# Performance work log

Measured on AMD Instinct MI355X. Metric: run time of the kernel, lower is better.

The kernel has to match this reference:

```python
import jax, jax.numpy as jnp
import numpy as np

B, N, E, H = 4, 2048, 512, 8
D = E // H  # head dim = 64


def setup_inputs() -> dict:
    key = jax.random.key(0)
    ks = jax.random.split(key, 5)
    s = 1.0 / np.sqrt(E)
    return {
        "x": jax.random.normal(ks[0], (B, N, E), dtype=jnp.float32),
        "Wk": jax.random.normal(ks[1], (E, E), dtype=jnp.float32) * s,
        "bk": jax.random.normal(ks[2], (E,), dtype=jnp.float32) * s,
        "Wv": jax.random.normal(ks[3], (E, E), dtype=jnp.float32) * s,
        "bv": jax.random.normal(ks[4], (E,), dtype=jnp.float32) * s,
    }


def reference(x, Wk, bk, Wv, bv):
    b, n, e = x.shape
    # Linear projections (torch Linear: y = x @ W.T + b), split into heads.
    keys = (x @ Wk.T + bk).reshape(b, n, H, D).transpose(0, 2, 1, 3)    # b h n d
    values = (x @ Wv.T + bv).reshape(b, n, H, D).transpose(0, 2, 1, 3)  # b h n d
    # Q = K self-attention: scores [b, h, n, n]
    dotprod = jnp.einsum('bhnd,bhmd->bhnm', keys, keys)
    # softmax over last axis, then unusual POST-softmax scaling by sqrt(emb)
    att = jax.nn.softmax(dotprod, axis=-1) / jnp.sqrt(jnp.asarray(e, x.dtype))
    # dropout p=0 -> identity
    out = jnp.einsum('bhnm,bhmd->bhnd', att, values)
    return out.transpose(0, 2, 1, 3).reshape(b, n, e)
```

## Files before the change

### kernel.cpp

```cpp
#include <hip/hip_runtime.h>

typedef __bf16 bf16_t;
typedef bf16_t bf16x8 __attribute__((ext_vector_type(8)));
typedef float f32x4 __attribute__((ext_vector_type(4)));

#define NSEQ 2048
#define EMB 512
#define HEADS 8
#define HD 64
#define BATCH 4
#define LOG2E 1.4426950408889634f

#define MFMA16(a, b, c) __builtin_amdgcn_mfma_f32_16x16x32_bf16(a, b, c, 0, 0, 0)

#define CX (BATCH * NSEQ * EMB / 8)
#define CW (EMB * EMB / 8)
__global__ __launch_bounds__(256) void convert_kernel(
    const float* __restrict__ x, const float* __restrict__ Wk,
    const float* __restrict__ Wv,
    bf16_t* __restrict__ xb, bf16_t* __restrict__ Wb)
{
  const int total = CX + 2 * CW;
  for (int c = blockIdx.x * 256 + threadIdx.x; c < total; c += gridDim.x * 256) {
    const float* src;
    bf16_t* dst;
    int off;
    if (c < CX)            { src = x;  dst = xb;      off = c; }
    else if (c < CX + CW)  { src = Wk; dst = Wb;      off = c - CX; }
    else                   { src = Wv; dst = Wb + (size_t)EMB * EMB; off = c - CX - CW; }
    const float4 a = *(const float4*)(src + (size_t)off * 8);
    const float4 bq = *(const float4*)(src + (size_t)off * 8 + 4);
    bf16x8 v;
    v[0] = (bf16_t)a.x;  v[1] = (bf16_t)a.y;  v[2] = (bf16_t)a.z;  v[3] = (bf16_t)a.w;
    v[4] = (bf16_t)bq.x; v[5] = (bf16_t)bq.y; v[6] = (bf16_t)bq.z; v[7] = (bf16_t)bq.w;
    *(bf16x8*)(dst + (size_t)off * 8) = v;
  }
}

__global__ __launch_bounds__(256, 2) void proj_kernel(
    const bf16_t* __restrict__ xb, const bf16_t* __restrict__ Wb,
    const float* __restrict__ bk, const float* __restrict__ bv,
    bf16_t* __restrict__ Kh, bf16_t* __restrict__ Vt)
{
  __shared__ union {
    struct {
      __align__(16) bf16_t A[2][128][40];
      __align__(16) bf16_t B[2][128][40];
    } s;
    __align__(16) bf16_t T[128][136];
  } u;

  const int t    = threadIdx.x;
  const int w    = t >> 6;
  const int lane = t & 63;
  const int quad = lane >> 4;
  const int l15  = lane & 15;
  const int wr   = w >> 1, wc = w & 1;
  const int m0   = blockIdx.x * 128;
  const int n0   = blockIdx.y * 128;
  const int zz   = (blockIdx.y >= 4);

  const int sr = t >> 3;
  const int sj = t & 7;
  const int sb = sj >> 2, sc = (sj & 3) * 8;

  bf16x8 pa[4], pb[4];
  auto prefetch = [&](int k0) {
#pragma unroll
    for (int i = 0; i < 4; ++i) {
      pa[i] = *(const bf16x8*)(xb + (size_t)(m0 + sr + i * 32) * EMB + k0 + sj * 8);
      pb[i] = *(const bf16x8*)(Wb + (size_t)(n0 + sr + i * 32) * EMB + k0 + sj * 8);
    }
  };

  f32x4 acc[4][4] = {};
  prefetch(0);

  for (int it = 0; it < 8; ++it) {
    __syncthreads();
#pragma unroll
    for (int i = 0; i < 4; ++i) {
      *(bf16x8*)(&u.s.A[sb][sr + i * 32][sc]) = pa[i];
      *(bf16x8*)(&u.s.B[sb][sr + i * 32][sc]) = pb[i];
    }
    __syncthreads();
    if (it < 7) prefetch((it + 1) * 64);

    bf16x8 af[4][2], bf[4][2];
#pragma unroll
    for (int mt = 0; mt < 4; ++mt)
#pragma unroll
      for (int kk = 0; kk < 2; ++kk)
        af[mt][kk] = *(const bf16x8*)(&u.s.A[kk][wr * 64 + mt * 16 + l15][quad * 8]);
#pragma unroll
    for (int nt = 0; nt < 4; ++nt)
#pragma unroll
      for (int kk = 0; kk < 2; ++kk)
        bf[nt][kk] = *(const bf16x8*)(&u.s.B[kk][wc * 64 + nt * 16 + l15][quad * 8]);
#pragma unroll
    for (int kk = 0; kk < 2; ++kk)
#pragma unroll
      for (int mt = 0; mt < 4; ++mt)
#pragma unroll
        for (int nt = 0; nt < 4; ++nt)
          acc[mt][nt] = MFMA16(af[mt][kk], bf[nt][kk], acc[mt][nt]);
  }

  __syncthreads();

#pragma unroll
  for (int mt = 0; mt < 4; ++mt) {
#pragma unroll
    for (int nt = 0; nt < 4; ++nt) {
      const int F = wc * 64 + nt * 16 + l15;
      const int c = n0 + F;
      const float bb = zz ? bv[c - 512] : bk[c];
#pragma unroll
      for (int reg = 0; reg < 4; ++reg) {
        const int R = wr * 64 + mt * 16 + quad * 4 + reg;
        const float v = acc[mt][nt][reg] + bb;
        if (!zz) u.T[R][F] = (bf16_t)v;
        else     u.T[F][R] = (bf16_t)v;
      }
    }
  }
  __syncthreads();

#pragma unroll
  for (int i = 0; i < 8; ++i) {
    const int q  = t + i * 256;
    const int R  = q >> 4;
    const int C8 = (q & 15) * 8;
    const bf16x8 v = *(const bf16x8*)(&u.T[R][C8]);
    if (!zz) {
      const int gr = m0 + R, b = gr >> 11, n = gr & (NSEQ - 1);
      const int c = n0 + C8, hh = c >> 6, d = c & 63;
      *(bf16x8*)(Kh + (((size_t)(b * HEADS + hh)) * NSEQ + n) * HD + d) = v;
    } else {
      const int cv = n0 + R - 512, hh = cv >> 6, d = cv & 63;
      const int gr = m0 + C8, b = gr >> 11, n = gr & (NSEQ - 1);
      *(bf16x8*)(Vt + (((size_t)(b * HEADS + hh)) * HD + d) * NSEQ + n) = v;
    }
  }
}

__global__ __launch_bounds__(256, 2) void flash_kernel(
    const bf16_t* __restrict__ Kh, const bf16_t* __restrict__ Vt,
    float* __restrict__ out)
{
  __shared__ __align__(16) bf16_t Kl[2][64][40];
  __shared__ __align__(16) bf16_t Vl[2][64][40];
  __shared__ __align__(16) bf16_t Pl[4][32][68];

  const int t    = threadIdx.x;
  const int w    = t >> 6;
  const int lane = t & 63;
  const int quad = lane >> 4;
  const int l15  = lane & 15;

  const int bh = blockIdx.x;
  const int b  = bh >> 3, h = bh & 7;
  const int rowbase = blockIdx.y * 128 + w * 32;

  const bf16_t* __restrict__ Kb = Kh + (size_t)bh * NSEQ * HD;
  const bf16_t* __restrict__ Vb = Vt + (size_t)bh * HD * NSEQ;

  bf16x8 qf[2][2];
#pragma unroll
  for (int mt = 0; mt < 2; ++mt)
#pragma unroll
    for (int kk = 0; kk < 2; ++kk)
      qf[mt][kk] = *(const bf16x8*)(Kb + (size_t)(rowbase + mt * 16 + l15) * HD +
                                    kk * 32 + quad * 8);

  float mlog[2][4];
#pragma unroll
  for (int mt = 0; mt < 2; ++mt) {
    float ss = 0.f;
#pragma unroll
    for (int kk = 0; kk < 2; ++kk)
#pragma unroll
      for (int j = 0; j < 8; ++j) {
        const float qv = (float)qf[mt][kk][j];
        ss = fmaf(qv, qv, ss);
      }
    ss += __shfl_xor(ss, 16, 64);
    ss += __shfl_xor(ss, 32, 64);
#pragma unroll
    for (int reg = 0; reg < 4; ++reg)
      mlog[mt][reg] =
          __shfl(ss, (lane & 48) | (((lane >> 4) << 2) + reg), 64) * LOG2E;
  }

  const int sr = t >> 3, sj = t & 7;
  const int sb = sj >> 2, sc = (sj & 3) * 8;

  bf16x8 pk[2], pv[2];
  auto prefetch = [&](int kt) {
    const bf16_t* Kt = Kb + (size_t)kt * 64 * HD;
    pk[0] = *(const bf16x8*)(Kt + (size_t)sr * HD + sj * 8);
    pk[1] = *(const bf16x8*)(Kt + (size_t)(sr + 32) * HD + sj * 8);
    pv[0] = *(const bf16x8*)(Vb + (size_t)sr * NSEQ + kt * 64 + sj * 8);
    pv[1] = *(const bf16x8*)(Vb + (size_t)(sr + 32) * NSEQ + kt * 64 + sj * 8);
  };

  f32x4 acco[2][4] = {};
  float lsum[2][4] = {};

  prefetch(0);

  for (int kt = 0; kt < NSEQ / 64; ++kt) {
    __syncthreads();
    *(bf16x8*)(&Kl[sb][sr][sc])      = pk[0];
    *(bf16x8*)(&Kl[sb][sr + 32][sc]) = pk[1];
    *(bf16x8*)(&Vl[sb][sr][sc])      = pv[0];
    *(bf16x8*)(&Vl[sb][sr + 32][sc]) = pv[1];
    __syncthreads();
    if (kt + 1 < NSEQ / 64) prefetch(kt + 1);

    bf16x8 kf[4][2];
#pragma unroll
    for (int nt = 0; nt < 4; ++nt)
#pragma unroll
      for (int kk = 0; kk < 2; ++kk)
        kf[nt][kk] = *(const bf16x8*)(&Kl[kk][nt * 16 + l15][quad * 8]);

    f32x4 s[2][4] = {};
#pragma unroll
    for (int mt = 0; mt < 2; ++mt)
#pragma unroll
      for (int nt = 0; nt < 4; ++nt) {
        s[mt][nt] = MFMA16(qf[mt][0], kf[nt][0], s[mt][nt]);
        s[mt][nt] = MFMA16(qf[mt][1], kf[nt][1], s[mt][nt]);
      }

#pragma unroll
    for (int mt = 0; mt < 2; ++mt)
#pragma unroll
      for (int nt = 0; nt < 4; ++nt)
#pragma unroll
        for (int reg = 0; reg < 4; ++reg) {
          const float p =
              __builtin_amdgcn_exp2f(fmaf(s[mt][nt][reg], LOG2E, -mlog[mt][reg]));
          lsum[mt][reg] += p;
          Pl[w][mt * 16 + quad * 4 + reg][nt * 16 + l15] = (bf16_t)p;
        }

#pragma unroll
    for (int kk = 0; kk < 2; ++kk) {
      bf16x8 vfs[4];
#pragma unroll
      for (int dt = 0; dt < 4; ++dt)
        vfs[dt] = *(const bf16x8*)(&Vl[kk][dt * 16 + l15][quad * 8]);
#pragma unroll
      for (int mt = 0; mt < 2; ++mt) {
        const bf16x8 pf =
            *(const bf16x8*)(&Pl[w][mt * 16 + l15][kk * 32 + quad * 8]);
#pragma unroll
        for (int dt = 0; dt < 4; ++dt)
          acco[mt][dt] = MFMA16(pf, vfs[dt], acco[mt][dt]);
      }
    }
  }

#pragma unroll
  for (int mt = 0; mt < 2; ++mt)
#pragma unroll
    for (int off = 1; off <= 8; off <<= 1)
#pragma unroll
      for (int reg = 0; reg < 4; ++reg)
        lsum[mt][reg] += __shfl_xor(lsum[mt][reg], off, 64);

  const float SCL = 0.044194173824159216f;
#pragma unroll
  for (int mt = 0; mt < 2; ++mt)
#pragma unroll
    for (int dt = 0; dt < 4; ++dt) {
      const int d = dt * 16 + l15;
#pragma unroll
      for (int reg = 0; reg < 4; ++reg) {
        const int n = rowbase + mt * 16 + quad * 4 + reg;
        const float f = SCL / lsum[mt][reg];
        out[((size_t)(b * NSEQ + n)) * EMB + h * HD + d] = acco[mt][dt][reg] * f;
      }
    }
}

extern "C" void kernel_launch(void* const* d_in, const int* in_sizes, int n_in,
                              void* d_out, int out_size, void* d_ws, size_t ws_size,
                              hipStream_t stream) {
  const float* x  = (const float*)d_in[0];
  const float* Wk = (const float*)d_in[1];
  const float* bk = (const float*)d_in[2];
  const float* Wv = (const float*)d_in[3];
  const float* bv = (const float*)d_in[4];
  float* out = (float*)d_out;

  bf16_t* Kh = (bf16_t*)d_ws;
  bf16_t* Vt = Kh + (size_t)BATCH * HEADS * NSEQ * HD;
  bf16_t* xb = Vt + (size_t)BATCH * HEADS * NSEQ * HD;
  bf16_t* Wb = xb + (size_t)BATCH * NSEQ * EMB;

  convert_kernel<<<1024, 256, 0, stream>>>(x, Wk, Wv, xb, Wb);

  dim3 pg(8192 / 128, 1024 / 128);
  proj_kernel<<<pg, 256, 0, stream>>>(xb, Wb, bk, bv, Kh, Vt);

  dim3 fg(BATCH * HEADS, NSEQ / 128);
  flash_kernel<<<fg, 256, 0, stream>>>(Kh, Vt, out);
}
```

Baseline: 147.9 us.

## Fuse fp32-to-bf16 conversion into projection; split flash keys across waves

Removes the separate conversion kernel: the projection kernel now loads fp32 x and weights directly and packs them to bf16 before staging in shared memory, which saves a launch and one round trip through memory for x. The flash kernel is restructured so each wave owns 64 query rows and half of each 64-key tile. It computes transposed scores (K·Q), keeps one row-max per lane, and writes P with packed 8-byte stores. A final shared-memory reduction merges the two key-halves' partial outputs and sums. The cost is doubled fp32 global read traffic in the projection, since x is re-read by every column block, plus a cross-wave reduction at the end.

Result: faster. 133.6 us (-9.7%).

```diff
diff --git a/kernel.cpp b/kernel.cpp
--- a/kernel.cpp
+++ b/kernel.cpp
@@ -13,33 +13,10 @@
 
 #define MFMA16(a, b, c) __builtin_amdgcn_mfma_f32_16x16x32_bf16(a, b, c, 0, 0, 0)
 
-#define CX (BATCH * NSEQ * EMB / 8)
-#define CW (EMB * EMB / 8)
-__global__ __launch_bounds__(256) void convert_kernel(
-    const float* __restrict__ x, const float* __restrict__ Wk,
-    const float* __restrict__ Wv,
-    bf16_t* __restrict__ xb, bf16_t* __restrict__ Wb)
-{
-  const int total = CX + 2 * CW;
-  for (int c = blockIdx.x * 256 + threadIdx.x; c < total; c += gridDim.x * 256) {
-    const float* src;
-    bf16_t* dst;
-    int off;
-    if (c < CX)            { src = x;  dst = xb;      off = c; }
-    else if (c < CX + CW)  { src = Wk; dst = Wb;      off = c - CX; }
-    else                   { src = Wv; dst = Wb + (size_t)EMB * EMB; off = c - CX - CW; }
-    const float4 a = *(const float4*)(src + (size_t)off * 8);
-    const float4 bq = *(const float4*)(src + (size_t)off * 8 + 4);
-    bf16x8 v;
-    v[0] = (bf16_t)a.x;  v[1] = (bf16_t)a.y;  v[2] = (bf16_t)a.z;  v[3] = (bf16_t)a.w;
-    v[4] = (bf16_t)bq.x; v[5] = (bf16_t)bq.y; v[6] = (bf16_t)bq.z; v[7] = (bf16_t)bq.w;
-    *(bf16x8*)(dst + (size_t)off * 8) = v;
-  }
-}
-
 __global__ __launch_bounds__(256, 2) void proj_kernel(
-    const bf16_t* __restrict__ xb, const bf16_t* __restrict__ Wb,
-    const float* __restrict__ bk, const float* __restrict__ bv,
+    const float* __restrict__ x,
+    const float* __restrict__ Wk, const float* __restrict__ bk,
+    const float* __restrict__ Wv, const float* __restrict__ bv,
     bf16_t* __restrict__ Kh, bf16_t* __restrict__ Vt)
 {
   __shared__ union {
@@ -59,18 +36,28 @@
   const int m0   = blockIdx.x * 128;
   const int n0   = blockIdx.y * 128;
   const int zz   = (blockIdx.y >= 4);
+  const float* __restrict__ W = zz ? Wv : Wk;
+  const int nW = n0 - zz * 512;
 
   const int sr = t >> 3;
   const int sj = t & 7;
   const int sb = sj >> 2, sc = (sj & 3) * 8;
 
-  bf16x8 pa[4], pb[4];
+  float4 pa[4][2], pb[4][2];
   auto prefetch = [&](int k0) {
 #pragma unroll
     for (int i = 0; i < 4; ++i) {
-      pa[i] = *(const bf16x8*)(xb + (size_t)(m0 + sr + i * 32) * EMB + k0 + sj * 8);
-      pb[i] = *(const bf16x8*)(Wb + (size_t)(n0 + sr + i * 32) * EMB + k0 + sj * 8);
-    }
+      const float* xa = x + (size_t)(m0 + sr + i * 32) * EMB + k0 + sj * 8;
+      const float* wa = W + (size_t)(nW + sr + i * 32) * EMB + k0 + sj * 8;
+      pa[i][0] = *(const float4*)xa; pa[i][1] = *(const float4*)(xa + 4);
+      pb[i][0] = *(const float4*)wa; pb[i][1] = *(const float4*)(wa + 4);
+    }
+  };
+  auto pack8 = [](float4 a, float4 b) -> bf16x8 {
+    bf16x8 v;
+    v[0] = (bf16_t)a.x; v[1] = (bf16_t)a.y; v[2] = (bf16_t)a.z; v[3] = (bf16_t)a.w;
+    v[4] = (bf16_t)b.x; v[5] = (bf16_t)b.y; v[6] = (bf16_t)b.z; v[7] = (bf16_t)b.w;
+    return v;
   };
 
   f32x4 acc[4][4] = {};
@@ -80,8 +67,8 @@
     __syncthreads();
 #pragma unroll
     for (int i = 0; i < 4; ++i) {
-      *(bf16x8*)(&u.s.A[sb][sr + i * 32][sc]) = pa[i];
-      *(bf16x8*)(&u.s.B[sb][sr + i * 32][sc]) = pb[i];
+      *(bf16x8*)(&u.s.A[sb][sr + i * 32][sc]) = pack8(pa[i][0], pa[i][1]);
+      *(bf16x8*)(&u.s.B[sb][sr + i * 32][sc]) = pack8(pb[i][0], pb[i][1]);
     }
     __syncthreads();
     if (it < 7) prefetch((it + 1) * 64);
@@ -148,48 +135,55 @@
     const bf16_t* __restrict__ Kh, const bf16_t* __restrict__ Vt,
     float* __restrict__ out)
 {
-  __shared__ __align__(16) bf16_t Kl[2][64][40];
-  __shared__ __align__(16) bf16_t Vl[2][64][40];
-  __shared__ __align__(16) bf16_t Pl[4][32][68];
+  __shared__ union {
+    struct {
+      __align__(16) bf16_t Kl[2][64][40];
+      __align__(16) bf16_t Vl[2][64][40];
+      __align__(16) bf16_t Pl[4][64][40];
+    } s;
+    struct {
+      __align__(16) float Cb[2][4096];
+      __align__(16) float Lb[2][64][4];
+    } c;
+  } u;
 
   const int t    = threadIdx.x;
   const int w    = t >> 6;
   const int lane = t & 63;
   const int quad = lane >> 4;
   const int l15  = lane & 15;
+  const int rh   = w & 1;
+  const int kh   = w >> 1;
 
   const int bh = blockIdx.x;
   const int b  = bh >> 3, h = bh & 7;
-  const int rowbase = blockIdx.y * 128 + w * 32;
+  const int rowbase = blockIdx.y * 128 + rh * 64;
 
   const bf16_t* __restrict__ Kb = Kh + (size_t)bh * NSEQ * HD;
   const bf16_t* __restrict__ Vb = Vt + (size_t)bh * HD * NSEQ;
 
-  bf16x8 qf[2][2];
-#pragma unroll
-  for (int mt = 0; mt < 2; ++mt)
+  bf16x8 qf[4][2];
+#pragma unroll
+  for (int nt = 0; nt < 4; ++nt)
 #pragma unroll
     for (int kk = 0; kk < 2; ++kk)
-      qf[mt][kk] = *(const bf16x8*)(Kb + (size_t)(rowbase + mt * 16 + l15) * HD +
+      qf[nt][kk] = *(const bf16x8*)(Kb + (size_t)(rowbase + nt * 16 + l15) * HD +
                                     kk * 32 + quad * 8);
 
-  float mlog[2][4];
-#pragma unroll
-  for (int mt = 0; mt < 2; ++mt) {
+  float mlog[4];
+#pragma unroll
+  for (int nt = 0; nt < 4; ++nt) {
     float ss = 0.f;
 #pragma unroll
     for (int kk = 0; kk < 2; ++kk)
 #pragma unroll
       for (int j = 0; j < 8; ++j) {
-        const float qv = (float)qf[mt][kk][j];
+        const float qv = (float)qf[nt][kk][j];
         ss = fmaf(qv, qv, ss);
       }
     ss += __shfl_xor(ss, 16, 64);
     ss += __shfl_xor(ss, 32, 64);
-#pragma unroll
-    for (int reg = 0; reg < 4; ++reg)
-      mlog[mt][reg] =
-          __shfl(ss, (lane & 48) | (((lane >> 4) << 2) + reg), 64) * LOG2E;
+    mlog[nt] = ss * LOG2E;
   }
 
   const int sr = t >> 3, sj = t & 7;
@@ -204,86 +198,105 @@
     pv[1] = *(const bf16x8*)(Vb + (size_t)(sr + 32) * NSEQ + kt * 64 + sj * 8);
   };
 
-  f32x4 acco[2][4] = {};
-  float lsum[2][4] = {};
+  f32x4 acco[4][4] = {};
+  float lsum[4] = {0.f, 0.f, 0.f, 0.f};
 
   prefetch(0);
 
   for (int kt = 0; kt < NSEQ / 64; ++kt) {
     __syncthreads();
-    *(bf16x8*)(&Kl[sb][sr][sc])      = pk[0];
-    *(bf16x8*)(&Kl[sb][sr + 32][sc]) = pk[1];
-    *(bf16x8*)(&Vl[sb][sr][sc])      = pv[0];
-    *(bf16x8*)(&Vl[sb][sr + 32][sc]) = pv[1];
+    *(bf16x8*)(&u.s.Kl[sb][sr][sc])      = pk[0];
+    *(bf16x8*)(&u.s.Kl[sb][sr + 32][sc]) = pk[1];
+    *(bf16x8*)(&u.s.Vl[sb][sr][sc])      = pv[0];
+    *(bf16x8*)(&u.s.Vl[sb][sr + 32][sc]) = pv[1];
     __syncthreads();
     if (kt + 1 < NSEQ / 64) prefetch(kt + 1);
 
-    bf16x8 kf[4][2];
-#pragma unroll
-    for (int nt = 0; nt < 4; ++nt)
+    bf16x8 kf[2][2];
+#pragma unroll
+    for (int jt = 0; jt < 2; ++jt)
 #pragma unroll
       for (int kk = 0; kk < 2; ++kk)
-        kf[nt][kk] = *(const bf16x8*)(&Kl[kk][nt * 16 + l15][quad * 8]);
-
-    f32x4 s[2][4] = {};
-#pragma unroll
-    for (int mt = 0; mt < 2; ++mt)
+        kf[jt][kk] =
+            *(const bf16x8*)(&u.s.Kl[kk][kh * 32 + jt * 16 + l15][quad * 8]);
+
+    f32x4 st[2][4] = {};
+#pragma unroll
+    for (int kk = 0; kk < 2; ++kk)
+#pragma unroll
+      for (int jt = 0; jt < 2; ++jt)
+#pragma unroll
+        for (int nt = 0; nt < 4; ++nt)
+          st[jt][nt] = MFMA16(kf[jt][kk], qf[nt][kk], st[jt][nt]);
+
+#pragma unroll
+    for (int jt = 0; jt < 2; ++jt)
 #pragma unroll
       for (int nt = 0; nt < 4; ++nt) {
-        s[mt][nt] = MFMA16(qf[mt][0], kf[nt][0], s[mt][nt]);
-        s[mt][nt] = MFMA16(qf[mt][1], kf[nt][1], s[mt][nt]);
-      }
-
-#pragma unroll
-    for (int mt = 0; mt < 2; ++mt)
-#pragma unroll
-      for (int nt = 0; nt < 4; ++nt)
+        union { bf16_t hx[4]; uint2 u2; } pw;
 #pragma unroll
         for (int reg = 0; reg < 4; ++reg) {
           const float p =
-              __builtin_amdgcn_exp2f(fmaf(s[mt][nt][reg], LOG2E, -mlog[mt][reg]));
-          lsum[mt][reg] += p;
-          Pl[w][mt * 16 + quad * 4 + reg][nt * 16 + l15] = (bf16_t)p;
+              __builtin_amdgcn_exp2f(fmaf(st[jt][nt][reg], LOG2E, -mlog[nt]));
+          lsum[nt] += p;
+          pw.hx[reg] = (bf16_t)p;
         }
-
-#pragma unroll
-    for (int kk = 0; kk < 2; ++kk) {
-      bf16x8 vfs[4];
+        *(uint2*)(&u.s.Pl[w][nt * 16 + l15][jt * 16 + quad * 4]) = pw.u2;
+      }
+
+    bf16x8 vf[4];
+#pragma unroll
+    for (int dt = 0; dt < 4; ++dt)
+      vf[dt] = *(const bf16x8*)(&u.s.Vl[kh][dt * 16 + l15][quad * 8]);
+#pragma unroll
+    for (int rt = 0; rt < 4; ++rt) {
+      const bf16x8 pf = *(const bf16x8*)(&u.s.Pl[w][rt * 16 + l15][quad * 8]);
 #pragma unroll
       for (int dt = 0; dt < 4; ++dt)
-        vfs[dt] = *(const bf16x8*)(&Vl[kk][dt * 16 + l15][quad * 8]);
-#pragma unroll
-      for (int mt = 0; mt < 2; ++mt) {
-        const bf16x8 pf =
-            *(const bf16x8*)(&Pl[w][mt * 16 + l15][kk * 32 + quad * 8]);
+        acco[rt][dt] = MFMA16(pf, vf[dt], acco[rt][dt]);
+    }
+  }
+
+  __syncthreads();
+  if (kh == 1) {
+#pragma unroll
+    for (int rt = 0; rt < 4; ++rt)
+#pragma unroll
+      for (int dt = 0; dt < 4; ++dt)
+        *(f32x4*)(&u.c.Cb[rh][((rt * 4 + dt) * 64 + lane) * 4]) = acco[rt][dt];
+#pragma unroll
+    for (int nt = 0; nt < 4; ++nt) u.c.Lb[rh][lane][nt] = lsum[nt];
+  }
+  __syncthreads();
+  if (kh == 0) {
+#pragma unroll
+    for (int rt = 0; rt < 4; ++rt)
+#pragma unroll
+      for (int dt = 0; dt < 4; ++dt) {
+        const f32x4 o = *(const f32x4*)(&u.c.Cb[rh][((rt * 4 + dt) * 64 + lane) * 4]);
+        acco[rt][dt] += o;
+      }
+#pragma unroll
+    for (int nt = 0; nt < 4; ++nt) {
+      lsum[nt] += u.c.Lb[rh][lane][nt];
+      lsum[nt] += __shfl_xor(lsum[nt], 16, 64);
+      lsum[nt] += __shfl_xor(lsum[nt], 32, 64);
+    }
+
+    const float SCL = 0.044194173824159216f;
+#pragma unroll
+    for (int rt = 0; rt < 4; ++rt)
+#pragma unroll
+      for (int reg = 0; reg < 4; ++reg) {
+        const float lr = __shfl(lsum[rt], quad * 4 + reg, 64);
+        const float f = SCL / lr;
+        const int n = rowbase + rt * 16 + quad * 4 + reg;
 #pragma unroll
         for (int dt = 0; dt < 4; ++dt)
-          acco[mt][dt] = MFMA16(pf, vfs[dt], acco[mt][dt]);
-      }
-    }
-  }
-
-#pragma unroll
-  for (int mt = 0; mt < 2; ++mt)
-#pragma unroll
-    for (int off = 1; off <= 8; off <<= 1)
-#pragma unroll
-      for (int reg = 0; reg < 4; ++reg)
-        lsum[mt][reg] += __shfl_xor(lsum[mt][reg], off, 64);
-
-  const float SCL = 0.044194173824159216f;
-#pragma unroll
-  for (int mt = 0; mt < 2; ++mt)
-#pragma unroll
-    for (int dt = 0; dt < 4; ++dt) {
-      const int d = dt * 16 + l15;
-#pragma unroll
-      for (int reg = 0; reg < 4; ++reg) {
-        const int n = rowbase + mt * 16 + quad * 4 + reg;
-        const float f = SCL / lsum[mt][reg];
-        out[((size_t)(b * NSEQ + n)) * EMB + h * HD + d] = acco[mt][dt][reg] * f;
-      }
-    }
+          out[((size_t)(b * NSEQ + n)) * EMB + h * HD + dt * 16 + l15] =
+              acco[rt][dt][reg] * f;
+      }
+  }
 }
 
 extern "C" void kernel_launch(void* const* d_in, const int* in_sizes, int n_in,
@@ -298,13 +311,9 @@
 
   bf16_t* Kh = (bf16_t*)d_ws;
   bf16_t* Vt = Kh + (size_t)BATCH * HEADS * NSEQ * HD;
-  bf16_t* xb = Vt + (size_t)BATCH * HEADS * NSEQ * HD;
-  bf16_t* Wb = xb + (size_t)BATCH * NSEQ * EMB;
-
-  convert_kernel<<<1024, 256, 0, stream>>>(x, Wk, Wv, xb, Wb);
 
   dim3 pg(8192 / 128, 1024 / 128);
-  proj_kernel<<<pg, 256, 0, stream>>>(xb, Wb, bk, bv, Kh, Vt);
+  proj_kernel<<<pg, 256, 0, stream>>>(x, Wk, bk, Wv, bv, Kh, Vt);
 
   dim3 fg(BATCH * HEADS, NSEQ / 128);
   flash_kernel<<<fg, 256, 0, stream>>>(Kh, Vt, out);
```
